# Optimization experiments

Hardware: AMD Instinct MI355X
Metric: run time of the kernel (lower is better)

Reference implementation:

```python
import jax, jax.numpy as jnp
import numpy as np
import math

NUM_HEADS = 16
HEAD_SIZE = 64
SEQ_LEN = 2048
D_MODEL = NUM_HEADS * HEAD_SIZE
BATCH = 2


def _xavier(key, shape):
    fan_in, fan_out = shape[0], shape[1]
    limit = math.sqrt(6.0 / (fan_in + fan_out))
    return jax.random.uniform(key, shape, jnp.float32, -limit, limit)


def setup_inputs() -> dict:
    key = jax.random.key(0)
    ks = jax.random.split(key, 5)
    x = jax.random.normal(ks[0], (BATCH, SEQ_LEN, D_MODEL), jnp.float32)
    W_Q = _xavier(ks[1], (D_MODEL, D_MODEL))
    W_K = _xavier(ks[2], (D_MODEL, D_MODEL))
    W_V = _xavier(ks[3], (D_MODEL, D_MODEL))
    W_O = _xavier(ks[4], (D_MODEL, D_MODEL))
    zeros = jnp.zeros((D_MODEL,), jnp.float32)
    return {
        "x": x,
        "W_Q": W_Q, "W_K": W_K, "W_V": W_V, "W_O": W_O,
        "b_Q": zeros, "b_K": zeros, "b_V": zeros, "b_O": zeros,
    }


def _split_heads(t):
    # [B, S, H*d] -> [B, H, S, d]
    B, S, _ = t.shape
    return t.reshape(B, S, NUM_HEADS, HEAD_SIZE).transpose(0, 2, 1, 3)


def reference(x, W_Q, W_K, W_V, W_O, b_Q, b_K, b_V, b_O):
    q = _split_heads(x @ W_Q + b_Q)  # [B,H,S,d]
    k = _split_heads(x @ W_K + b_K)
    v = _split_heads(x @ W_V + b_V)

    # scores: [B,H,S,S]
    scores = jnp.einsum("bhqd,bhkd->bhqk", q, k)
    # Faithful to original: multiply by lower-triangular 0/1 mask, scale,
    # then add -10000 on strictly-upper positions (NOT -inf).
    tril = jnp.tril(jnp.ones((SEQ_LEN, SEQ_LEN), jnp.float32))
    neg_bias = jnp.triu(jnp.full((SEQ_LEN, SEQ_LEN), -10000.0, jnp.float32), 1)
    masked = scores * tril / np.sqrt(HEAD_SIZE).astype(np.float32) + neg_bias
    weights = jax.nn.softmax(masked, axis=-1)

    hs = jnp.einsum("bhqk,bhkd->bhqd", weights, v)  # [B,H,S,d]
    B = hs.shape[0]
    merged = hs.transpose(0, 2, 1, 3).reshape(B, SEQ_LEN, D_MODEL)
    return merged @ W_O + b_O
```

## Files before the change

### kernel.cpp

```cpp
#include <hip/hip_runtime.h>
#include <hip/hip_bf16.h>

#define S_LEN 2048
#define NH 16
#define HD 64
#define DM 1024
#define BATCH 2
#define M_ROWS (BATCH * S_LEN)
#define SCALE2 0.18033688011112043f
#define M2FIX 8.0f

typedef float f32x4 __attribute__((ext_vector_type(4)));
typedef __bf16 bf16x8 __attribute__((ext_vector_type(8)));
typedef short short8 __attribute__((ext_vector_type(8)));

__device__ __forceinline__ unsigned short f2bf(float f) {
  unsigned u = __builtin_bit_cast(unsigned, f);
  u += 0x7FFFu + ((u >> 16) & 1u);
  return (unsigned short)(u >> 16);
}

__device__ __forceinline__ f32x4 mfma16(bf16x8 a, bf16x8 b, f32x4 c) {
  return __builtin_amdgcn_mfma_f32_16x16x32_bf16(a, b, c, 0, 0, 0);
}

__device__ __forceinline__ void gload_lds16(const void* g, void* l) {
  __builtin_amdgcn_global_load_lds(
      (const __attribute__((address_space(1))) void*)g,
      (__attribute__((address_space(3))) void*)l, 16, 0, 0);
}

__global__ __launch_bounds__(256) void cast_bf16_kernel(
    const float* __restrict__ in, unsigned short* __restrict__ out) {
  int i = blockIdx.x * 256 + threadIdx.x;
  const float4* p = (const float4*)in;
  float4 f0 = p[i * 2], f1 = p[i * 2 + 1];
  short8 o;
  o[0] = (short)f2bf(f0.x); o[1] = (short)f2bf(f0.y);
  o[2] = (short)f2bf(f0.z); o[3] = (short)f2bf(f0.w);
  o[4] = (short)f2bf(f1.x); o[5] = (short)f2bf(f1.y);
  o[6] = (short)f2bf(f1.z); o[7] = (short)f2bf(f1.w);
  ((short8*)out)[i] = o;
}

__global__ __launch_bounds__(256) void transpose_cast_kernel(
    const float* __restrict__ W0, const float* __restrict__ W1,
    const float* __restrict__ W2, const float* __restrict__ W3,
    unsigned short* __restrict__ out) {
  int z = blockIdx.z;
  const float* W = (z == 0) ? W0 : (z == 1) ? W1 : (z == 2) ? W2 : W3;
  __shared__ float tile[32][33];
  int tx = threadIdx.x & 31, ty = threadIdx.x >> 5;
  int bx = blockIdx.x * 32, by = blockIdx.y * 32;
#pragma unroll
  for (int i = 0; i < 4; ++i)
    tile[ty + i * 8][tx] = W[(size_t)(by + ty + i * 8) * DM + bx + tx];
  __syncthreads();
  unsigned short* o = out + (size_t)z * DM * DM;
#pragma unroll
  for (int i = 0; i < 4; ++i)
    o[(size_t)(bx + ty + i * 8) * DM + by + tx] = f2bf(tile[tx][ty + i * 8]);
}

template <int MODE>
__global__ __launch_bounds__(256) void gemm_bt_kernel(
    const unsigned short* __restrict__ A, const unsigned short* __restrict__ Bt,
    void* __restrict__ Cptr, const float* __restrict__ bias0,
    const float* __restrict__ bias1, const float* __restrict__ bias2,
    int M, int N, int K) {
  __shared__ __align__(16) unsigned short Sbuf[2][3][4096];
  unsigned short (*As)[4096] = Sbuf[0];
  unsigned short (*Bs)[4096] = Sbuf[1];
  const int t = threadIdx.x, lane = t & 63;
  const int wid = t >> 6, wr = wid >> 1, wc = wid & 1;
  const int r16 = lane & 15, g = lane >> 4;
  const int m0 = blockIdx.y * 128, n0 = blockIdx.x * 128;
  const int nk = K >> 5;

  const int n1 = t, n2 = t + 256;
  const int r1g = t >> 2, c1g = (t & 3) * 8;
  const int r2g = (t + 256) >> 2;

  const unsigned short* ap1 = A + (size_t)(m0 + r1g) * K + c1g;
  const unsigned short* ap2 = A + (size_t)(m0 + r2g) * K + c1g;
  const unsigned short* bp1 = Bt + (size_t)(n0 + r1g) * K + c1g;
  const unsigned short* bp2 = Bt + (size_t)(n0 + r2g) * K + c1g;

#define GSTAGE(s)                          \
  gload_lds16(ap1, &As[s][n1 * 8]);        \
  gload_lds16(bp1, &Bs[s][n1 * 8]);        \
  gload_lds16(ap2, &As[s][n2 * 8]);        \
  gload_lds16(bp2, &Bs[s][n2 * 8]);        \
  ap1 += 32; ap2 += 32; bp1 += 32; bp2 += 32;

  f32x4 acc[4][4] = {};

  GSTAGE(0);
  GSTAGE(1);

  for (int kt = 0; kt < nk; ++kt) {
    const int cs = kt % 3;
    if (kt + 1 < nk) {
      asm volatile("s_waitcnt vmcnt(4)" ::: "memory");
    } else {
      asm volatile("s_waitcnt vmcnt(0)" ::: "memory");
    }
    __builtin_amdgcn_s_barrier();
    if (kt + 2 < nk) { GSTAGE((kt + 2) % 3); }

    bf16x8 af[4], bfr[4];
#pragma unroll
    for (int mi = 0; mi < 4; ++mi)
      af[mi] = *(const bf16x8*)&As[cs][(wr * 64 + mi * 16 + r16) * 32 + g * 8];
#pragma unroll
    for (int ni = 0; ni < 4; ++ni)
      bfr[ni] = *(const bf16x8*)&Bs[cs][(wc * 64 + ni * 16 + r16) * 32 + g * 8];
    __builtin_amdgcn_s_setprio(1);
#pragma unroll
    for (int mi = 0; mi < 4; ++mi)
#pragma unroll
      for (int ni = 0; ni < 4; ++ni)
        acc[mi][ni] = mfma16(af[mi], bfr[ni], acc[mi][ni]);
    __builtin_amdgcn_s_setprio(0);
  }
#undef GSTAGE

  if (MODE == 0) {
    unsigned short* Cb = (unsigned short*)Cptr;
    const int buf = n0 >> 10;
    if (buf < 2) {
      const float* bp = buf ? bias1 : bias0;
      const float sc = buf ? 1.0f : SCALE2;
#pragma unroll
      for (int ni = 0; ni < 4; ++ni) {
        int cn = (n0 & 1023) + wc * 64 + ni * 16 + r16;
        float bv = bp[cn];
#pragma unroll
        for (int mi = 0; mi < 4; ++mi) {
          int rowb = m0 + wr * 64 + mi * 16 + 4 * g;
#pragma unroll
          for (int j = 0; j < 4; ++j)
            Cb[(size_t)buf * 4194304u + (size_t)(rowb + j) * 1024 + cn] =
                __builtin_bit_cast(unsigned short, (__bf16)((acc[mi][ni][j] + bv) * sc));
        }
      }
    } else {
      unsigned short* T = &Sbuf[0][0][0];
      __syncthreads();
#pragma unroll
      for (int ni = 0; ni < 4; ++ni) {
        int cnl = wc * 64 + ni * 16 + r16;
        float bv = bias2[(n0 & 1023) + cnl];
#pragma unroll
        for (int mi = 0; mi < 4; ++mi) {
          int sl = wr * 64 + mi * 16 + 4 * g;
          union { __bf16 h4[4]; uint2 u; } cv;
#pragma unroll
          for (int j = 0; j < 4; ++j) cv.h4[j] = (__bf16)(acc[mi][ni][j] + bv);
          *(uint2*)&T[cnl * 136 + sl] = cv.u;
        }
      }
      __syncthreads();
      const int bb = m0 >> 11, s0g = m0 & 2047;
      unsigned short* Vt = Cb + 8388608u;
#pragma unroll
      for (int p = 0; p < 8; ++p) {
        int idx = p * 256 + t;
        int cnl = idx >> 4, sch = idx & 15;
        int cng = (n0 & 1023) + cnl;
        int hh = cng >> 6, d = cng & 63;
        short8 v = *(const short8*)&T[cnl * 136 + sch * 8];
        *(short8*)&Vt[(((size_t)((bb * 16 + hh) * 64 + d)) << 11) + s0g + sch * 8] = v;
      }
    }
  } else {
    float* Cf = (float*)Cptr;
#pragma unroll
    for (int ni = 0; ni < 4; ++ni) {
      int col = n0 + wc * 64 + ni * 16 + r16;
      float bv = bias0[col];
#pragma unroll
      for (int mi = 0; mi < 4; ++mi) {
        int rowb = m0 + wr * 64 + mi * 16 + 4 * g;
#pragma unroll
        for (int j = 0; j < 4; ++j)
          Cf[(size_t)(rowb + j) * N + col] = acc[mi][ni][j] + bv;
      }
    }
  }
}

__global__ __launch_bounds__(256) void attn_kernel(
    const unsigned short* __restrict__ Qm, const unsigned short* __restrict__ Km,
    const unsigned short* __restrict__ VtG, unsigned short* __restrict__ Om) {
  const int t = threadIdx.x, lane = t & 63, w = t >> 6;
  const int r16 = lane & 15, g = lane >> 4;
  const int bid = blockIdx.x;
  const int xk = bid & 7, slot = bid >> 3;
  const int grp = xk + 8 * (slot >> 4);
  const int mq = slot & 15;
  const int h = grp & 15, b = grp >> 4;

  __shared__ __align__(16) unsigned short Ks[3][4096];
  __shared__ __align__(16) unsigned short Vs[3][4096];
  __shared__ __align__(16) unsigned short Pl[4608];

  const unsigned short* Kbase = Km + (size_t)(b * S_LEN) * DM + h * HD;
  const unsigned short* Vbase = VtG + (size_t)((b * NH + h) * HD) * S_LEN;

  const int n1 = t, n2 = t + 256;
  const int r1 = n1 >> 3, c1 = ((n1 & 7) ^ (r1 & 7)) * 8;
  const int r2 = n2 >> 3, c2 = ((n2 & 7) ^ (r2 & 7)) * 8;
  const int sx = r16 & 7;
  const int qloc = w * 16 + r16;

  unsigned short* Pw = &Pl[w * 1152];
  unsigned* Pw32 = (unsigned*)Pw;

#define STAGE(s)                          \
  gload_lds16(kp1, &Ks[s][n1 * 8]);       \
  gload_lds16(kp2, &Ks[s][n2 * 8]);       \
  gload_lds16(vp1, &Vs[s][n1 * 8]);       \
  gload_lds16(vp2, &Vs[s][n2 * 8]);       \
  kp1 += 64 * DM; kp2 += 64 * DM; vp1 += 64; vp2 += 64;

  for (int half = 0; half < 2; ++half) {
    const int qt = half ? 31 - mq : mq;
    const int q0 = qt * 64;
    const unsigned short* Qp = Qm + (size_t)(b * S_LEN + q0 + qloc) * DM + h * HD;
    bf16x8 qf0 = *(const bf16x8*)(Qp + g * 8);
    bf16x8 qf1 = *(const bf16x8*)(Qp + 32 + g * 8);

    f32x4 oacc[4] = {};
    float lsum = 0.f;
    const int ntk = qt + 1;

    const unsigned short* kp1 = Kbase + (size_t)r1 * DM + c1;
    const unsigned short* kp2 = Kbase + (size_t)r2 * DM + c2;
    const unsigned short* vp1 = Vbase + (size_t)r1 * S_LEN + c1;
    const unsigned short* vp2 = Vbase + (size_t)r2 * S_LEN + c2;

    __syncthreads();
    STAGE(0);
    STAGE(1);

    for (int kt = 0; kt < ntk; ++kt) {
      const int cs = kt % 3;
      if (kt + 1 < ntk) {
        asm volatile("s_waitcnt vmcnt(4)" ::: "memory");
      } else {
        asm volatile("s_waitcnt vmcnt(0)" ::: "memory");
      }
      __builtin_amdgcn_s_barrier();
      if (kt + 2 < ntk) { STAGE((kt + 2) % 3); }

      f32x4 st[4];
#pragma unroll
      for (int ni = 0; ni < 4; ++ni) {
        int row = ni * 16 + r16;
        f32x4 z = {};
        bf16x8 kf0 = *(const bf16x8*)&Ks[cs][row * 64 + ((g ^ sx) * 8)];
        bf16x8 kf1 = *(const bf16x8*)&Ks[cs][row * 64 + (((4 + g) ^ sx) * 8)];
        __builtin_amdgcn_s_setprio(1);
        st[ni] = mfma16(kf1, qf1, mfma16(kf0, qf0, z));
        __builtin_amdgcn_s_setprio(0);
      }

      float p[4][4];
#pragma unroll
      for (int ni = 0; ni < 4; ++ni)
#pragma unroll
        for (int j = 0; j < 4; ++j)
          p[ni][j] = __builtin_amdgcn_exp2f(st[ni][j] - M2FIX);
      if (kt == qt) {
#pragma unroll
        for (int ni = 0; ni < 4; ++ni)
#pragma unroll
          for (int j = 0; j < 4; ++j) {
            int kvl = ni * 16 + 4 * g + j;
            if (kvl > qloc) p[ni][j] = 0.f;
          }
      }
      lsum += ((p[0][0] + p[0][1]) + (p[0][2] + p[0][3])) +
              ((p[1][0] + p[1][1]) + (p[1][2] + p[1][3])) +
              ((p[2][0] + p[2][1]) + (p[2][2] + p[2][3])) +
              ((p[3][0] + p[3][1]) + (p[3][2] + p[3][3]));

#pragma unroll
      for (int ni = 0; ni < 4; ++ni) {
        union { __bf16 hh[4]; uint2 u; } cv;
        cv.hh[0] = (__bf16)p[ni][0];
        cv.hh[1] = (__bf16)p[ni][1];
        cv.hh[2] = (__bf16)p[ni][2];
        cv.hh[3] = (__bf16)p[ni][3];
        *(uint2*)&Pw32[r16 * 36 + ni * 8 + 2 * g] = cv.u;
      }
      bf16x8 pf0 = *(const bf16x8*)&Pw[r16 * 72 + g * 8];
      bf16x8 pf1 = *(const bf16x8*)&Pw[r16 * 72 + 32 + g * 8];

      __builtin_amdgcn_s_setprio(1);
#pragma unroll
      for (int di = 0; di < 4; ++di) {
        int row = di * 16 + r16;
        bf16x8 vf0 = *(const bf16x8*)&Vs[cs][row * 64 + ((g ^ sx) * 8)];
        bf16x8 vf1 = *(const bf16x8*)&Vs[cs][row * 64 + (((4 + g) ^ sx) * 8)];
        oacc[di] = mfma16(vf0, pf0, oacc[di]);
        oacc[di] = mfma16(vf1, pf1, oacc[di]);
      }
      __builtin_amdgcn_s_setprio(0);
    }

    lsum += __shfl_xor(lsum, 16);
    lsum += __shfl_xor(lsum, 32);
    float li = 1.0f / lsum;
    unsigned short* op = Om + (size_t)(b * S_LEN + q0 + qloc) * DM + h * HD;
#pragma unroll
    for (int di = 0; di < 4; ++di) {
      union { __bf16 hh[4]; uint2 u; } ov;
      ov.hh[0] = (__bf16)(oacc[di][0] * li);
      ov.hh[1] = (__bf16)(oacc[di][1] * li);
      ov.hh[2] = (__bf16)(oacc[di][2] * li);
      ov.hh[3] = (__bf16)(oacc[di][3] * li);
      *(uint2*)(op + di * 16 + 4 * g) = ov.u;
    }
  }
#undef STAGE
}

extern "C" void kernel_launch(void* const* d_in, const int* in_sizes, int n_in,
                              void* d_out, int out_size, void* d_ws, size_t ws_size,
                              hipStream_t stream) {
  (void)in_sizes; (void)n_in; (void)out_size; (void)ws_size;
  const float* x  = (const float*)d_in[0];
  const float* WQ = (const float*)d_in[1];
  const float* WK = (const float*)d_in[2];
  const float* WV = (const float*)d_in[3];
  const float* WO = (const float*)d_in[4];
  const float* bQ = (const float*)d_in[5];
  const float* bK = (const float*)d_in[6];
  const float* bV = (const float*)d_in[7];
  const float* bO = (const float*)d_in[8];

  char* ws = (char*)d_ws;
  unsigned short* xb  = (unsigned short*)(ws);
  unsigned short* wt  = (unsigned short*)(ws + (8u << 20));
  unsigned short* qb  = (unsigned short*)(ws + (16u << 20));
  unsigned short* hsb = (unsigned short*)(ws + (40u << 20));

  cast_bf16_kernel<<<2048, 256, 0, stream>>>(x, xb);
  transpose_cast_kernel<<<dim3(32, 32, 4), 256, 0, stream>>>(WQ, WK, WV, WO, wt);
  gemm_bt_kernel<0><<<dim3(24, 32), 256, 0, stream>>>(
      xb, wt, (void*)qb, bQ, bK, bV, M_ROWS, 3072, DM);
  attn_kernel<<<512, 256, 0, stream>>>(qb, qb + 4194304u, qb + 8388608u, hsb);
  gemm_bt_kernel<1><<<dim3(8, 32), 256, 0, stream>>>(
      hsb, wt + 3u * 1048576u, d_out, bO, nullptr, nullptr, M_ROWS, DM, DM);
}
```

Before: 107.3 us.

## Stage 128-key tiles with double buffering instead of triple-buffered 64-key tiles

The attention kernel now loads K and V in 128-key tiles into two LDS buffers instead of 64-key tiles into three. Each tile is processed as two 64-key sub-steps, and the V layout and its swizzle are changed to 128-wide rows. This halves the number of barriers and wait points per query tile. In exchange, each wait drains all outstanding loads (vmcnt(0)) with only one tile in flight, so prefetch overlap is shallower. Some wasted loads can occur on the diagonal tile when its second half is skipped.

```diff
diff --git a/kernel.cpp b/kernel.cpp
--- a/kernel.cpp
+++ b/kernel.cpp
@@ -201,28 +201,30 @@
   const int mq = slot & 15;
   const int h = grp & 15, b = grp >> 4;
 
-  __shared__ __align__(16) unsigned short Ks[3][4096];
-  __shared__ __align__(16) unsigned short Vs[3][4096];
+  __shared__ __align__(16) unsigned short Ks[2][8192];
+  __shared__ __align__(16) unsigned short Vs[2][8192];
   __shared__ __align__(16) unsigned short Pl[4608];
 
   const unsigned short* Kbase = Km + (size_t)(b * S_LEN) * DM + h * HD;
   const unsigned short* Vbase = VtG + (size_t)((b * NH + h) * HD) * S_LEN;
 
-  const int n1 = t, n2 = t + 256;
-  const int r1 = n1 >> 3, c1 = ((n1 & 7) ^ (r1 & 7)) * 8;
-  const int r2 = n2 >> 3, c2 = ((n2 & 7) ^ (r2 & 7)) * 8;
-  const int sx = r16 & 7;
+  const int kc = ((t & 7) ^ ((t >> 3) & 7)) * 8;
+  const int vc = ((t & 15) ^ (t >> 4)) * 8;
+  const unsigned short* kp = Kbase + (size_t)(t >> 3) * DM + kc;
+  const unsigned short* vp = Vbase + (size_t)(t >> 4) * S_LEN + vc;
+  const int sxk = r16 & 7;
   const int qloc = w * 16 + r16;
 
   unsigned short* Pw = &Pl[w * 1152];
   unsigned* Pw32 = (unsigned*)Pw;
 
-#define STAGE(s)                          \
-  gload_lds16(kp1, &Ks[s][n1 * 8]);       \
-  gload_lds16(kp2, &Ks[s][n2 * 8]);       \
-  gload_lds16(vp1, &Vs[s][n1 * 8]);       \
-  gload_lds16(vp2, &Vs[s][n2 * 8]);       \
-  kp1 += 64 * DM; kp2 += 64 * DM; vp1 += 64; vp2 += 64;
+#define STAGE(s, kv0)                                                          \
+  do {                                                                         \
+    _Pragma("unroll") for (int p = 0; p < 4; ++p)                              \
+        gload_lds16(kp + (size_t)((kv0) + 32 * p) * DM, &Ks[s][(t + 256 * p) * 8]); \
+    _Pragma("unroll") for (int p = 0; p < 4; ++p)                              \
+        gload_lds16(vp + (size_t)(16 * p) * S_LEN + (kv0), &Vs[s][(t + 256 * p) * 8]); \
+  } while (0)
 
   for (int half = 0; half < 2; ++half) {
     const int qt = half ? 31 - mq : mq;
@@ -233,81 +235,78 @@
 
     f32x4 oacc[4] = {};
     float lsum = 0.f;
-    const int ntk = qt + 1;
-
-    const unsigned short* kp1 = Kbase + (size_t)r1 * DM + c1;
-    const unsigned short* kp2 = Kbase + (size_t)r2 * DM + c2;
-    const unsigned short* vp1 = Vbase + (size_t)r1 * S_LEN + c1;
-    const unsigned short* vp2 = Vbase + (size_t)r2 * S_LEN + c2;
+    const int nt2 = (qt + 2) >> 1;
 
     __syncthreads();
-    STAGE(0);
-    STAGE(1);
-
-    for (int kt = 0; kt < ntk; ++kt) {
-      const int cs = kt % 3;
-      if (kt + 1 < ntk) {
-        asm volatile("s_waitcnt vmcnt(4)" ::: "memory");
-      } else {
-        asm volatile("s_waitcnt vmcnt(0)" ::: "memory");
-      }
+    STAGE(0, 0);
+
+    for (int kt = 0; kt < nt2; ++kt) {
+      const int cs = kt & 1;
+      asm volatile("s_waitcnt vmcnt(0)" ::: "memory");
       __builtin_amdgcn_s_barrier();
-      if (kt + 2 < ntk) { STAGE((kt + 2) % 3); }
-
-      f32x4 st[4];
-#pragma unroll
-      for (int ni = 0; ni < 4; ++ni) {
-        int row = ni * 16 + r16;
-        f32x4 z = {};
-        bf16x8 kf0 = *(const bf16x8*)&Ks[cs][row * 64 + ((g ^ sx) * 8)];
-        bf16x8 kf1 = *(const bf16x8*)&Ks[cs][row * 64 + (((4 + g) ^ sx) * 8)];
+      if (kt + 1 < nt2) { STAGE(cs ^ 1, (kt + 1) * 128); }
+
+      const int kvbase = kt * 128;
+#pragma unroll
+      for (int u = 0; u < 2; ++u) {
+        const int kvs = kvbase + u * 64;
+        if (kvs > q0 + 63) break;
+
+        f32x4 st[4];
+#pragma unroll
+        for (int ni = 0; ni < 4; ++ni) {
+          int row = u * 64 + ni * 16 + r16;
+          f32x4 z = {};
+          bf16x8 kf0 = *(const bf16x8*)&Ks[cs][row * 64 + ((g ^ sxk) * 8)];
+          bf16x8 kf1 = *(const bf16x8*)&Ks[cs][row * 64 + (((4 + g) ^ sxk) * 8)];
+          __builtin_amdgcn_s_setprio(1);
+          st[ni] = mfma16(kf1, qf1, mfma16(kf0, qf0, z));
+          __builtin_amdgcn_s_setprio(0);
+        }
+
+        float p[4][4];
+#pragma unroll
+        for (int ni = 0; ni < 4; ++ni)
+#pragma unroll
+          for (int j = 0; j < 4; ++j)
+            p[ni][j] = __builtin_amdgcn_exp2f(st[ni][j] - M2FIX);
+        if (kvs == q0) {
+#pragma unroll
+          for (int ni = 0; ni < 4; ++ni)
+#pragma unroll
+            for (int j = 0; j < 4; ++j) {
+              int kvl = ni * 16 + 4 * g + j;
+              if (kvl > qloc) p[ni][j] = 0.f;
+            }
+        }
+        lsum += ((p[0][0] + p[0][1]) + (p[0][2] + p[0][3])) +
+                ((p[1][0] + p[1][1]) + (p[1][2] + p[1][3])) +
+                ((p[2][0] + p[2][1]) + (p[2][2] + p[2][3])) +
+                ((p[3][0] + p[3][1]) + (p[3][2] + p[3][3]));
+
+#pragma unroll
+        for (int ni = 0; ni < 4; ++ni) {
+          union { __bf16 hh[4]; uint2 u2; } cv;
+          cv.hh[0] = (__bf16)p[ni][0];
+          cv.hh[1] = (__bf16)p[ni][1];
+          cv.hh[2] = (__bf16)p[ni][2];
+          cv.hh[3] = (__bf16)p[ni][3];
+          *(uint2*)&Pw32[r16 * 36 + ni * 8 + 2 * g] = cv.u2;
+        }
+        bf16x8 pf0 = *(const bf16x8*)&Pw[r16 * 72 + g * 8];
+        bf16x8 pf1 = *(const bf16x8*)&Pw[r16 * 72 + 32 + g * 8];
+
         __builtin_amdgcn_s_setprio(1);
-        st[ni] = mfma16(kf1, qf1, mfma16(kf0, qf0, z));
+#pragma unroll
+        for (int di = 0; di < 4; ++di) {
+          int row = di * 16 + r16;
+          bf16x8 vf0 = *(const bf16x8*)&Vs[cs][row * 128 + (((u * 8 + g) ^ r16) * 8)];
+          bf16x8 vf1 = *(const bf16x8*)&Vs[cs][row * 128 + (((u * 8 + 4 + g) ^ r16) * 8)];
+          oacc[di] = mfma16(vf0, pf0, oacc[di]);
+          oacc[di] = mfma16(vf1, pf1, oacc[di]);
+        }
         __builtin_amdgcn_s_setprio(0);
       }
-
-      float p[4][4];
-#pragma unroll
-      for (int ni = 0; ni < 4; ++ni)
-#pragma unroll
-        for (int j = 0; j < 4; ++j)
-          p[ni][j] = __builtin_amdgcn_exp2f(st[ni][j] - M2FIX);
-      if (kt == qt) {
-#pragma unroll
-        for (int ni = 0; ni < 4; ++ni)
-#pragma unroll
-          for (int j = 0; j < 4; ++j) {
-            int kvl = ni * 16 + 4 * g + j;
-            if (kvl > qloc) p[ni][j] = 0.f;
-          }
-      }
-      lsum += ((p[0][0] + p[0][1]) + (p[0][2] + p[0][3])) +
-              ((p[1][0] + p[1][1]) + (p[1][2] + p[1][3])) +
-              ((p[2][0] + p[2][1]) + (p[2][2] + p[2][3])) +
-              ((p[3][0] + p[3][1]) + (p[3][2] + p[3][3]));
-
-#pragma unroll
-      for (int ni = 0; ni < 4; ++ni) {
-        union { __bf16 hh[4]; uint2 u; } cv;
-        cv.hh[0] = (__bf16)p[ni][0];
-        cv.hh[1] = (__bf16)p[ni][1];
-        cv.hh[2] = (__bf16)p[ni][2];
-        cv.hh[3] = (__bf16)p[ni][3];
-        *(uint2*)&Pw32[r16 * 36 + ni * 8 + 2 * g] = cv.u;
-      }
-      bf16x8 pf0 = *(const bf16x8*)&Pw[r16 * 72 + g * 8];
-      bf16x8 pf1 = *(const bf16x8*)&Pw[r16 * 72 + 32 + g * 8];
-
-      __builtin_amdgcn_s_setprio(1);
-#pragma unroll
-      for (int di = 0; di < 4; ++di) {
-        int row = di * 16 + r16;
-        bf16x8 vf0 = *(const bf16x8*)&Vs[cs][row * 64 + ((g ^ sx) * 8)];
-        bf16x8 vf1 = *(const bf16x8*)&Vs[cs][row * 64 + (((4 + g) ^ sx) * 8)];
-        oacc[di] = mfma16(vf0, pf0, oacc[di]);
-        oacc[di] = mfma16(vf1, pf1, oacc[di]);
-      }
-      __builtin_amdgcn_s_setprio(0);
     }
 
     lsum += __shfl_xor(lsum, 16);
@@ -316,12 +315,12 @@
     unsigned short* op = Om + (size_t)(b * S_LEN + q0 + qloc) * DM + h * HD;
 #pragma unroll
     for (int di = 0; di < 4; ++di) {
-      union { __bf16 hh[4]; uint2 u; } ov;
+      union { __bf16 hh[4]; uint2 u2; } ov;
       ov.hh[0] = (__bf16)(oacc[di][0] * li);
       ov.hh[1] = (__bf16)(oacc[di][1] * li);
       ov.hh[2] = (__bf16)(oacc[di][2] * li);
       ov.hh[3] = (__bf16)(oacc[di][3] * li);
-      *(uint2*)(op + di * 16 + 4 * g) = ov.u;
+      *(uint2*)(op + di * 16 + 4 * g) = ov.u2;
     }
   }
 #undef STAGE
```

Measured after the change: 105.6 us. About the same (-1.6%).

## Split attention into one q-tile per block and drop triple-buffered K/V staging

Applied to the files above, without the earlier changes.

The attention launch grows from 512 to 1024 blocks, each handling a single 64-row query tile instead of a paired light/heavy tile. The three-stage async K/V ring buffer is replaced by a single buffer that loads, waits fully and uses barriers on every iteration, which shrinks LDS use so more blocks can be resident. The row-sum is now computed with an MFMA against a ones vector rather than per-lane adds plus shuffles. The cost is that load latency is no longer hidden inside a block and the per-block causal work is now unbalanced, so the design leans on higher occupancy to overlap memory and compute.

```diff
diff --git a/kernel.cpp b/kernel.cpp
--- a/kernel.cpp
+++ b/kernel.cpp
@@ -196,14 +196,15 @@
   const int t = threadIdx.x, lane = t & 63, w = t >> 6;
   const int r16 = lane & 15, g = lane >> 4;
   const int bid = blockIdx.x;
-  const int xk = bid & 7, slot = bid >> 3;
-  const int grp = xk + 8 * (slot >> 4);
-  const int mq = slot & 15;
+  const int xk = bid & 7, s = bid >> 3;
+  const int grp = xk * 4 + (s >> 5);
+  const int ss = s & 31;
+  const int qt = (ss & 1) ? (ss >> 1) : (31 - (ss >> 1));
   const int h = grp & 15, b = grp >> 4;
 
-  __shared__ __align__(16) unsigned short Ks[3][4096];
-  __shared__ __align__(16) unsigned short Vs[3][4096];
-  __shared__ __align__(16) unsigned short Pl[4608];
+  __shared__ __align__(16) unsigned short Ks[4096];
+  __shared__ __align__(16) unsigned short Vs[4096];
+  __shared__ __align__(16) unsigned short Pl[4][1152];
 
   const unsigned short* Kbase = Km + (size_t)(b * S_LEN) * DM + h * HD;
   const unsigned short* Vbase = VtG + (size_t)((b * NH + h) * HD) * S_LEN;
@@ -213,118 +214,104 @@
   const int r2 = n2 >> 3, c2 = ((n2 & 7) ^ (r2 & 7)) * 8;
   const int sx = r16 & 7;
   const int qloc = w * 16 + r16;
-
-  unsigned short* Pw = &Pl[w * 1152];
+  const int q0 = qt * 64;
+
+  unsigned short* Pw = Pl[w];
   unsigned* Pw32 = (unsigned*)Pw;
 
-#define STAGE(s)                          \
-  gload_lds16(kp1, &Ks[s][n1 * 8]);       \
-  gload_lds16(kp2, &Ks[s][n2 * 8]);       \
-  gload_lds16(vp1, &Vs[s][n1 * 8]);       \
-  gload_lds16(vp2, &Vs[s][n2 * 8]);       \
-  kp1 += 64 * DM; kp2 += 64 * DM; vp1 += 64; vp2 += 64;
-
-  for (int half = 0; half < 2; ++half) {
-    const int qt = half ? 31 - mq : mq;
-    const int q0 = qt * 64;
-    const unsigned short* Qp = Qm + (size_t)(b * S_LEN + q0 + qloc) * DM + h * HD;
-    bf16x8 qf0 = *(const bf16x8*)(Qp + g * 8);
-    bf16x8 qf1 = *(const bf16x8*)(Qp + 32 + g * 8);
-
-    f32x4 oacc[4] = {};
-    float lsum = 0.f;
-    const int ntk = qt + 1;
-
-    const unsigned short* kp1 = Kbase + (size_t)r1 * DM + c1;
-    const unsigned short* kp2 = Kbase + (size_t)r2 * DM + c2;
-    const unsigned short* vp1 = Vbase + (size_t)r1 * S_LEN + c1;
-    const unsigned short* vp2 = Vbase + (size_t)r2 * S_LEN + c2;
-
-    __syncthreads();
-    STAGE(0);
-    STAGE(1);
-
-    for (int kt = 0; kt < ntk; ++kt) {
-      const int cs = kt % 3;
-      if (kt + 1 < ntk) {
-        asm volatile("s_waitcnt vmcnt(4)" ::: "memory");
-      } else {
-        asm volatile("s_waitcnt vmcnt(0)" ::: "memory");
-      }
-      __builtin_amdgcn_s_barrier();
-      if (kt + 2 < ntk) { STAGE((kt + 2) % 3); }
-
-      f32x4 st[4];
-#pragma unroll
-      for (int ni = 0; ni < 4; ++ni) {
-        int row = ni * 16 + r16;
-        f32x4 z = {};
-        bf16x8 kf0 = *(const bf16x8*)&Ks[cs][row * 64 + ((g ^ sx) * 8)];
-        bf16x8 kf1 = *(const bf16x8*)&Ks[cs][row * 64 + (((4 + g) ^ sx) * 8)];
-        __builtin_amdgcn_s_setprio(1);
-        st[ni] = mfma16(kf1, qf1, mfma16(kf0, qf0, z));
-        __builtin_amdgcn_s_setprio(0);
-      }
-
-      float p[4][4];
+  const unsigned short* Qp = Qm + (size_t)(b * S_LEN + q0 + qloc) * DM + h * HD;
+  bf16x8 qf0 = *(const bf16x8*)(Qp + g * 8);
+  bf16x8 qf1 = *(const bf16x8*)(Qp + 32 + g * 8);
+
+  bf16x8 ones;
+#pragma unroll
+  for (int e = 0; e < 8; ++e) ones[e] = (__bf16)1.0f;
+
+  f32x4 oacc[4] = {};
+  f32x4 lacc = {};
+  const int ntk = qt + 1;
+
+  const unsigned short* kp1 = Kbase + (size_t)r1 * DM + c1;
+  const unsigned short* kp2 = Kbase + (size_t)r2 * DM + c2;
+  const unsigned short* vp1 = Vbase + (size_t)r1 * S_LEN + c1;
+  const unsigned short* vp2 = Vbase + (size_t)r2 * S_LEN + c2;
+
+  for (int kt = 0; kt < ntk; ++kt) {
+    gload_lds16(kp1, &Ks[n1 * 8]);
+    gload_lds16(kp2, &Ks[n2 * 8]);
+    gload_lds16(vp1, &Vs[n1 * 8]);
+    gload_lds16(vp2, &Vs[n2 * 8]);
+    kp1 += 64 * DM; kp2 += 64 * DM; vp1 += 64; vp2 += 64;
+    asm volatile("s_waitcnt vmcnt(0)" ::: "memory");
+    __builtin_amdgcn_s_barrier();
+
+    f32x4 st[4];
+#pragma unroll
+    for (int ni = 0; ni < 4; ++ni) {
+      int row = ni * 16 + r16;
+      f32x4 z = {};
+      bf16x8 kf0 = *(const bf16x8*)&Ks[row * 64 + ((g ^ sx) * 8)];
+      bf16x8 kf1 = *(const bf16x8*)&Ks[row * 64 + (((4 + g) ^ sx) * 8)];
+      __builtin_amdgcn_s_setprio(1);
+      st[ni] = mfma16(kf1, qf1, mfma16(kf0, qf0, z));
+      __builtin_amdgcn_s_setprio(0);
+    }
+
+    float p[4][4];
+#pragma unroll
+    for (int ni = 0; ni < 4; ++ni)
+#pragma unroll
+      for (int j = 0; j < 4; ++j)
+        p[ni][j] = __builtin_amdgcn_exp2f(st[ni][j] - M2FIX);
+    if (kt == qt) {
 #pragma unroll
       for (int ni = 0; ni < 4; ++ni)
 #pragma unroll
-        for (int j = 0; j < 4; ++j)
-          p[ni][j] = __builtin_amdgcn_exp2f(st[ni][j] - M2FIX);
-      if (kt == qt) {
-#pragma unroll
-        for (int ni = 0; ni < 4; ++ni)
-#pragma unroll
-          for (int j = 0; j < 4; ++j) {
-            int kvl = ni * 16 + 4 * g + j;
-            if (kvl > qloc) p[ni][j] = 0.f;
-          }
-      }
-      lsum += ((p[0][0] + p[0][1]) + (p[0][2] + p[0][3])) +
-              ((p[1][0] + p[1][1]) + (p[1][2] + p[1][3])) +
-              ((p[2][0] + p[2][1]) + (p[2][2] + p[2][3])) +
-              ((p[3][0] + p[3][1]) + (p[3][2] + p[3][3]));
-
-#pragma unroll
-      for (int ni = 0; ni < 4; ++ni) {
-        union { __bf16 hh[4]; uint2 u; } cv;
-        cv.hh[0] = (__bf16)p[ni][0];
-        cv.hh[1] = (__bf16)p[ni][1];
-        cv.hh[2] = (__bf16)p[ni][2];
-        cv.hh[3] = (__bf16)p[ni][3];
-        *(uint2*)&Pw32[r16 * 36 + ni * 8 + 2 * g] = cv.u;
-      }
-      bf16x8 pf0 = *(const bf16x8*)&Pw[r16 * 72 + g * 8];
-      bf16x8 pf1 = *(const bf16x8*)&Pw[r16 * 72 + 32 + g * 8];
-
-      __builtin_amdgcn_s_setprio(1);
-#pragma unroll
-      for (int di = 0; di < 4; ++di) {
-        int row = di * 16 + r16;
-        bf16x8 vf0 = *(const bf16x8*)&Vs[cs][row * 64 + ((g ^ sx) * 8)];
-        bf16x8 vf1 = *(const bf16x8*)&Vs[cs][row * 64 + (((4 + g) ^ sx) * 8)];
-        oacc[di] = mfma16(vf0, pf0, oacc[di]);
-        oacc[di] = mfma16(vf1, pf1, oacc[di]);
-      }
-      __builtin_amdgcn_s_setprio(0);
-    }
-
-    lsum += __shfl_xor(lsum, 16);
-    lsum += __shfl_xor(lsum, 32);
-    float li = 1.0f / lsum;
-    unsigned short* op = Om + (size_t)(b * S_LEN + q0 + qloc) * DM + h * HD;
+        for (int j = 0; j < 4; ++j) {
+          int kvl = ni * 16 + 4 * g + j;
+          if (kvl > qloc) p[ni][j] = 0.f;
+        }
+    }
+
+#pragma unroll
+    for (int ni = 0; ni < 4; ++ni) {
+      union { __bf16 hh[4]; uint2 u2; } cv;
+      cv.hh[0] = (__bf16)p[ni][0];
+      cv.hh[1] = (__bf16)p[ni][1];
+      cv.hh[2] = (__bf16)p[ni][2];
+      cv.hh[3] = (__bf16)p[ni][3];
+      *(uint2*)&Pw32[r16 * 36 + ni * 8 + 2 * g] = cv.u2;
+    }
+    bf16x8 pf0 = *(const bf16x8*)&Pw[r16 * 72 + g * 8];
+    bf16x8 pf1 = *(const bf16x8*)&Pw[r16 * 72 + 32 + g * 8];
+
+    lacc = mfma16(ones, pf1, mfma16(ones, pf0, lacc));
+
+    __builtin_amdgcn_s_setprio(1);
 #pragma unroll
     for (int di = 0; di < 4; ++di) {
-      union { __bf16 hh[4]; uint2 u; } ov;
-      ov.hh[0] = (__bf16)(oacc[di][0] * li);
-      ov.hh[1] = (__bf16)(oacc[di][1] * li);
-      ov.hh[2] = (__bf16)(oacc[di][2] * li);
-      ov.hh[3] = (__bf16)(oacc[di][3] * li);
-      *(uint2*)(op + di * 16 + 4 * g) = ov.u;
-    }
+      int row = di * 16 + r16;
+      bf16x8 vf0 = *(const bf16x8*)&Vs[row * 64 + ((g ^ sx) * 8)];
+      bf16x8 vf1 = *(const bf16x8*)&Vs[row * 64 + (((4 + g) ^ sx) * 8)];
+      oacc[di] = mfma16(vf0, pf0, oacc[di]);
+      oacc[di] = mfma16(vf1, pf1, oacc[di]);
+    }
+    __builtin_amdgcn_s_setprio(0);
+
+    __builtin_amdgcn_s_barrier();
   }
-#undef STAGE
+
+  float li = 1.0f / lacc[0];
+  unsigned short* op = Om + (size_t)(b * S_LEN + q0 + qloc) * DM + h * HD;
+#pragma unroll
+  for (int di = 0; di < 4; ++di) {
+    union { __bf16 hh[4]; uint2 u2; } ov;
+    ov.hh[0] = (__bf16)(oacc[di][0] * li);
+    ov.hh[1] = (__bf16)(oacc[di][1] * li);
+    ov.hh[2] = (__bf16)(oacc[di][2] * li);
+    ov.hh[3] = (__bf16)(oacc[di][3] * li);
+    *(uint2*)(op + di * 16 + 4 * g) = ov.u2;
+  }
 }
 
 extern "C" void kernel_launch(void* const* d_in, const int* in_sizes, int n_in,
@@ -351,7 +338,7 @@
   transpose_cast_kernel<<<dim3(32, 32, 4), 256, 0, stream>>>(WQ, WK, WV, WO, wt);
   gemm_bt_kernel<0><<<dim3(24, 32), 256, 0, stream>>>(
       xb, wt, (void*)qb, bQ, bK, bV, M_ROWS, 3072, DM);
-  attn_kernel<<<512, 256, 0, stream>>>(qb, qb + 4194304u, qb + 8388608u, hsb);
+  attn_kernel<<<1024, 256, 0, stream>>>(qb, qb + 4194304u, qb + 8388608u, hsb);
   gemm_bt_kernel<1><<<dim3(8, 32), 256, 0, stream>>>(
       hsb, wt + 3u * 1048576u, d_out, bO, nullptr, nullptr, M_ROWS, DM, DM);
 }
```

Result: slower. 120.0 us (+11.8%).
